# Kernel optimization log

Hardware: AMD Instinct MI355X
Metric: run time of the kernel (lower is better)

## Reference

```python
import jax, jax.numpy as jnp
import numpy as np

B, T, D, H = 4, 2048, 1024, 16
HD = D // H  # 64
LOCAL_CTX, BLOCKSIZE, VERTSIZE = 256, 1, 16
STRIDE = LOCAL_CTX // BLOCKSIZE  # 256


def build_fixed_mask(n):
    # num_verts == 1 branch of generate_fixed_attention_mask
    layout = np.zeros((n, n), dtype=np.bool_)
    # vertical stripes: top `vertsize` indices of each stride block
    for idx in range(STRIDE - VERTSIZE, STRIDE):
        layout[:, idx::STRIDE] = True
    rows = np.arange(n)
    # local: each query attends to its own stride-block
    same_block = (rows[:, None] // STRIDE) == (rows[None, :] // STRIDE)
    layout |= same_block
    # causal: zero out k > q
    layout &= rows[None, :] <= rows[:, None]
    return layout


def setup_inputs() -> dict:
    key = jax.random.key(0)
    k1, k2, k3, k4, k5 = jax.random.split(key, 5)
    s = 0.02
    return {
        "x": jax.random.normal(k1, (B, T, D), dtype=jnp.float32),
        "Wqkv": jax.random.normal(k2, (D, 3 * D), dtype=jnp.float32) * s,
        "bqkv": jax.random.normal(k3, (3 * D,), dtype=jnp.float32) * s,
        "Wproj": jax.random.normal(k4, (D, D), dtype=jnp.float32) * s,
        "bproj": jax.random.normal(k5, (D,), dtype=jnp.float32) * s,
        "mask": jnp.asarray(build_fixed_mask(T)),
    }


def reference(x, Wqkv, bqkv, Wproj, bproj, mask):
    b, t, _ = x.shape
    qkv = (x @ Wqkv + bqkv).reshape(b, t, 3, H, HD)
    # (B,T,3,H,HD) -> (B,H,T,HD) per component
    q = qkv[:, :, 0].transpose(0, 2, 1, 3)
    k = qkv[:, :, 1].transpose(0, 2, 1, 3)
    v = qkv[:, :, 2].transpose(0, 2, 1, 3)
    att = jnp.einsum("bhqd,bhkd->bhqk", q, k) * (1.0 / jnp.sqrt(jnp.float32(HD)))
    att = jnp.where(mask[:t, :t], att, -jnp.inf)
    att = jax.nn.softmax(att, axis=-1)
    y = jnp.einsum("bhqk,bhkd->bhqd", att, v)
    y = y.transpose(0, 2, 1, 3).reshape(b, t, D)
    return y @ Wproj + bproj
```

## Files before the change

kernel.cpp:

```cpp
#include <hip/hip_runtime.h>
#include <cstdint>
#include <cstddef>

typedef unsigned short u16;
typedef __attribute__((ext_vector_type(8))) short short8;
typedef __attribute__((ext_vector_type(4))) float f32x4;
typedef __attribute__((ext_vector_type(4))) unsigned short u16x4;

#define B_ 4
#define T_ 2048
#define D_ 1024
#define H_ 16
#define HD_ 64

__device__ __forceinline__ u16 f2bf(float f) {
  union { float f; unsigned i; } v; v.f = f;
  unsigned r = (v.i + 0x7FFFu + ((v.i >> 16) & 1u)) >> 16;
  return (u16)r;
}

__device__ __forceinline__ void load_lds16(const void* g, void* l) {
  __builtin_amdgcn_global_load_lds(
      (const __attribute__((address_space(1))) void*)g,
      (__attribute__((address_space(3))) void*)l, 16, 0, 0);
}

__global__ __launch_bounds__(256) void cvt_f32_bf16(const float* __restrict__ src,
                                                    u16* __restrict__ dst) {
  const size_t i = ((size_t)blockIdx.x * 256 + threadIdx.x) * 4;
  const f32x4 v = *(const f32x4*)(src + i);
  u16x4 o;
#pragma unroll
  for (int r = 0; r < 4; ++r) o[r] = f2bf(v[r]);
  *(u16x4*)(dst + i) = o;
}

__global__ __launch_bounds__(256) void transpose_cvt(const float* __restrict__ src,
                                                     u16* __restrict__ dst,
                                                     int R, int C) {
  __shared__ u16 t[32][33];
  const int c0 = blockIdx.x * 32, r0 = blockIdx.y * 32;
  const int tid = threadIdx.x;
  const int lr = tid >> 5, lc = tid & 31;
#pragma unroll
  for (int p = 0; p < 4; ++p)
    t[lr + p * 8][lc] = f2bf(src[(size_t)(r0 + lr + p * 8) * C + c0 + lc]);
  __syncthreads();
#pragma unroll
  for (int p = 0; p < 4; ++p)
    dst[(size_t)(c0 + lr + p * 8) * R + r0 + lc] = t[lc][lr + p * 8];
}

template <int EPI>
__global__ __launch_bounds__(256)
void gemm_bt(const u16* __restrict__ A, const u16* __restrict__ Bt,
             const float* __restrict__ bias, int K, int N,
             void* __restrict__ o0v, u16* __restrict__ o1, u16* __restrict__ o2) {
  __shared__ u16 As[128 * 32];
  __shared__ u16 Bs[128 * 32];
  const int tid = threadIdx.x;
  const int lane = tid & 63;
  const int w = tid >> 6;
  const int q = lane >> 4, col = lane & 15;
  const int m0 = blockIdx.y * 128, n0 = blockIdx.x * 128;
  const int wm = (w >> 1) * 64, wn = (w & 1) * 64;
  const int srow = tid >> 2, soff = (tid & 3) * 8;

  f32x4 acc[4][4] = {};

  const u16* Ap = A + (size_t)(m0 + srow) * K + soff;
  const u16* Bp = Bt + (size_t)(n0 + srow) * K + soff;

  for (int kb = 0; kb < K; kb += 32) {
    load_lds16(Ap + kb, &As[tid * 8]);
    load_lds16(Ap + (size_t)64 * K + kb, &As[2048 + tid * 8]);
    load_lds16(Bp + kb, &Bs[tid * 8]);
    load_lds16(Bp + (size_t)64 * K + kb, &Bs[2048 + tid * 8]);
    __syncthreads();
    short8 af[4], bfr[4];
#pragma unroll
    for (int i = 0; i < 4; ++i)
      af[i] = *(const short8*)&As[(wm + i * 16 + col) * 32 + q * 8];
#pragma unroll
    for (int j = 0; j < 4; ++j)
      bfr[j] = *(const short8*)&Bs[(wn + j * 16 + col) * 32 + q * 8];
#pragma unroll
    for (int i = 0; i < 4; ++i)
#pragma unroll
      for (int j = 0; j < 4; ++j)
        acc[i][j] = __builtin_amdgcn_mfma_f32_16x16x32_bf16(af[i], bfr[j], acc[i][j], 0, 0, 0);
    __syncthreads();
  }

#pragma unroll
  for (int j = 0; j < 4; ++j) {
    const int n = n0 + wn + j * 16 + col;
    const float bv = bias[n];
    if constexpr (EPI == 0) {
      u16* q0p = (u16*)o0v;
      const int c = n >> 10, rem = n & 1023, hh = rem >> 6, dd = rem & 63;
#pragma unroll
      for (int i = 0; i < 4; ++i) {
        const int mrow = m0 + wm + i * 16 + q * 4;
        const int b = mrow >> 11, t = mrow & 2047;
        const int bh = b * H_ + hh;
        if (c == 0) {
#pragma unroll
          for (int r = 0; r < 4; ++r)
            q0p[((size_t)bh * T_ + t + r) * HD_ + dd] = f2bf((acc[i][j][r] + bv) * 0.125f);
        } else if (c == 1) {
#pragma unroll
          for (int r = 0; r < 4; ++r)
            o1[((size_t)bh * T_ + t + r) * HD_ + dd] = f2bf(acc[i][j][r] + bv);
        } else {
          u16x4 pk;
#pragma unroll
          for (int r = 0; r < 4; ++r) pk[r] = f2bf(acc[i][j][r] + bv);
          *(u16x4*)&o2[((size_t)bh * HD_ + dd) * T_ + t] = pk;
        }
      }
    } else {
      float* outp = (float*)o0v;
#pragma unroll
      for (int i = 0; i < 4; ++i) {
        const int mrow = m0 + wm + i * 16 + q * 4;
#pragma unroll
        for (int r = 0; r < 4; ++r)
          outp[(size_t)(mrow + r) * N + n] = acc[i][j][r] + bv;
      }
    }
  }
}

__global__ __launch_bounds__(256)
void sparse_attn(const u16* __restrict__ Qb, const u16* __restrict__ Kb,
                 const u16* __restrict__ Vt, u16* __restrict__ Y) {
  __shared__ char smem[20480];
  u16* Pall = (u16*)smem;
  float* Obuf = (float*)smem;

  const int tid = threadIdx.x, lane = tid & 63, w = tid >> 6;
  const int q = lane >> 4, col = lane & 15;
  const int bh = blockIdx.y, qt = blockIdx.x;
  const int b = bh >> 4, hh = bh & 15;
  const int qb = qt >> 2;
  const int rb = (qt & 3) * 64;
  const int qg = qt * 64;
  const u16* Qh = Qb + (size_t)bh * T_ * HD_;
  const u16* Kh = Kb + (size_t)bh * T_ * HD_;
  const u16* Vh = Vt + (size_t)bh * HD_ * T_;

  short8 qf[4][2];
#pragma unroll
  for (int i = 0; i < 4; ++i)
#pragma unroll
    for (int h2 = 0; h2 < 2; ++h2)
      qf[i][h2] = *(const short8*)&Qh[(size_t)(qg + i * 16 + col) * HD_ + h2 * 32 + q * 8];

  f32x4 o[4][4] = {};
  f32x4 lI[4] = {};
  const short8 ones = {0x3F80, 0x3F80, 0x3F80, 0x3F80, 0x3F80, 0x3F80, 0x3F80, 0x3F80};

  u16* P = Pall + w * 2560;

  const int ns = (qb + 1) >> 1;
  const int L = ns + 2 * (qt & 3) + 2;

  for (int j = w; j < L; j += 4) {
    int k0, k1, localc;
    bool mask1;
    if (j < ns) {
      k0 = (2 * j) * 256 + 240; k1 = k0 + 256;
      mask1 = (2 * j + 1 == qb); localc = -1;
    } else {
      const int c = j - ns;
      k0 = qb * 256 + c * 32; k1 = k0 + 16;
      mask1 = false; localc = c * 32;
    }
    short8 k0a = *(const short8*)&Kh[(size_t)(k0 + col) * HD_ + q * 8];
    short8 k0b = *(const short8*)&Kh[(size_t)(k0 + col) * HD_ + 32 + q * 8];
    short8 k1a = *(const short8*)&Kh[(size_t)(k1 + col) * HD_ + q * 8];
    short8 k1b = *(const short8*)&Kh[(size_t)(k1 + col) * HD_ + 32 + q * 8];
#pragma unroll
    for (int rt = 0; rt < 4; ++rt) {
      f32x4 z = {0.f, 0.f, 0.f, 0.f};
      f32x4 s0 = __builtin_amdgcn_mfma_f32_16x16x32_bf16(qf[rt][0], k0a, z, 0, 0, 0);
      s0 = __builtin_amdgcn_mfma_f32_16x16x32_bf16(qf[rt][1], k0b, s0, 0, 0, 0);
      f32x4 s1 = __builtin_amdgcn_mfma_f32_16x16x32_bf16(qf[rt][0], k1a, z, 0, 0, 0);
      s1 = __builtin_amdgcn_mfma_f32_16x16x32_bf16(qf[rt][1], k1b, s1, 0, 0, 0);
#pragma unroll
      for (int r = 0; r < 4; ++r) {
        float p0 = __expf(s0[r]);
        float p1 = mask1 ? 0.f : __expf(s1[r]);
        if (localc >= 0) {
          const int qr = rb + rt * 16 + q * 4 + r;
          if (localc + col > qr) p0 = 0.f;
          if (localc + 16 + col > qr) p1 = 0.f;
        }
        P[(rt * 16 + q * 4 + r) * 40 + col] = f2bf(p0);
        P[(rt * 16 + q * 4 + r) * 40 + 16 + col] = f2bf(p1);
      }
    }
    asm volatile("s_waitcnt lgkmcnt(0)" ::: "memory");
    short8 pf[4], vf[4];
#pragma unroll
    for (int rt = 0; rt < 4; ++rt)
      pf[rt] = *(const short8*)&P[(rt * 16 + col) * 40 + q * 8];
    const int kvb = (q < 2) ? (k0 + q * 8) : (k1 + (q - 2) * 8);
#pragma unroll
    for (int dt = 0; dt < 4; ++dt)
      vf[dt] = *(const short8*)&Vh[(size_t)(dt * 16 + col) * T_ + kvb];
#pragma unroll
    for (int rt = 0; rt < 4; ++rt) {
#pragma unroll
      for (int dt = 0; dt < 4; ++dt)
        o[rt][dt] = __builtin_amdgcn_mfma_f32_16x16x32_bf16(pf[rt], vf[dt], o[rt][dt], 0, 0, 0);
      lI[rt] = __builtin_amdgcn_mfma_f32_16x16x32_bf16(pf[rt], ones, lI[rt], 0, 0, 0);
    }
  }

#pragma unroll
  for (int rt = 0; rt < 4; ++rt) {
    __syncthreads();
#pragma unroll
    for (int dt = 0; dt < 4; ++dt)
      *(f32x4*)&Obuf[(w * 65 + dt * 16 + col) * 16 + q * 4] = o[rt][dt];
    if (col == 0)
      *(f32x4*)&Obuf[(w * 65 + 64) * 16 + q * 4] = lI[rt];
    __syncthreads();
    f32x4 acc = {0.f, 0.f, 0.f, 0.f};
    f32x4 lt = {0.f, 0.f, 0.f, 0.f};
#pragma unroll
    for (int w2 = 0; w2 < 4; ++w2) {
      acc += *(const f32x4*)&Obuf[(w2 * 65 + w * 16 + col) * 16 + q * 4];
      lt += *(const f32x4*)&Obuf[(w2 * 65 + 64) * 16 + q * 4];
    }
#pragma unroll
    for (int r = 0; r < 4; ++r) {
      const int trow = qg + rt * 16 + q * 4 + r;
      Y[((size_t)(b * T_ + trow)) * D_ + hh * HD_ + w * 16 + col] = f2bf(acc[r] / lt[r]);
    }
  }
}

extern "C" void kernel_launch(void* const* d_in, const int* in_sizes, int n_in,
                              void* d_out, int out_size, void* d_ws, size_t ws_size,
                              hipStream_t stream) {
  const float* x = (const float*)d_in[0];
  const float* Wqkv = (const float*)d_in[1];
  const float* bqkv = (const float*)d_in[2];
  const float* Wproj = (const float*)d_in[3];
  const float* bproj = (const float*)d_in[4];
  float* out = (float*)d_out;

  char* ws = (char*)d_ws;
  u16* xb     = (u16*)(ws + 0);
  u16* WqkvT  = (u16*)(ws + 16777216);
  u16* WprojT = (u16*)(ws + 23068672);
  u16* Qb     = (u16*)(ws + 25165824);
  u16* Kb     = (u16*)(ws + 41943040);
  u16* Vt     = (u16*)(ws + 58720256);
  u16* Y      = (u16*)(ws + 75497472);

  cvt_f32_bf16<<<dim3(8192), 256, 0, stream>>>(x, xb);
  transpose_cvt<<<dim3(96, 32), 256, 0, stream>>>(Wqkv, WqkvT, 1024, 3072);
  transpose_cvt<<<dim3(32, 32), 256, 0, stream>>>(Wproj, WprojT, 1024, 1024);
  gemm_bt<0><<<dim3(24, 64), 256, 0, stream>>>(xb, WqkvT, bqkv, 1024, 3072, Qb, Kb, Vt);
  sparse_attn<<<dim3(32, 64), 256, 0, stream>>>(Qb, Kb, Vt, Y);
  gemm_bt<1><<<dim3(8, 64), 256, 0, stream>>>(Y, WprojT, bproj, 1024, 1024, out, nullptr, nullptr);
}
```

Measured before the change: 271.7 us.

## Replace GEMM with 256x256-tile, 4-stage LDS pipelined, swizzled MFMA kernel

Rewrites both projection GEMMs to use 256x256 output tiles with 512 threads. It uses a 4-buffer LDS ring that prefetches three K-tiles ahead via global_load_lds with fine-grained vmcnt waits, and XOR-swizzles LDS columns to avoid bank conflicts. Each wave computes a 128x64 sub-tile, with MFMA sections given raised priority. The aim is to hide global load latency and raise data reuse. In exchange it uses 128KB of LDS and many more accumulator registers, and produces fewer blocks (384 and 128), which may underfill the 256 CUs for the output projection.

```diff
diff --git a/kernel.cpp b/kernel.cpp
--- a/kernel.cpp
+++ b/kernel.cpp
@@ -52,45 +52,90 @@
 }
 
 template <int EPI>
-__global__ __launch_bounds__(256)
-void gemm_bt(const u16* __restrict__ A, const u16* __restrict__ Bt,
+__global__ __launch_bounds__(512, 2)
+void gemm256(const u16* __restrict__ A, const u16* __restrict__ Bt,
              const float* __restrict__ bias, int K, int N,
              void* __restrict__ o0v, u16* __restrict__ o1, u16* __restrict__ o2) {
-  __shared__ u16 As[128 * 32];
-  __shared__ u16 Bs[128 * 32];
+  __shared__ u16 tbuf[4 * 16384];
   const int tid = threadIdx.x;
   const int lane = tid & 63;
   const int w = tid >> 6;
   const int q = lane >> 4, col = lane & 15;
-  const int m0 = blockIdx.y * 128, n0 = blockIdx.x * 128;
-  const int wm = (w >> 1) * 64, wn = (w & 1) * 64;
-  const int srow = tid >> 2, soff = (tid & 3) * 8;
-
-  f32x4 acc[4][4] = {};
-
-  const u16* Ap = A + (size_t)(m0 + srow) * K + soff;
-  const u16* Bp = Bt + (size_t)(n0 + srow) * K + soff;
-
-  for (int kb = 0; kb < K; kb += 32) {
-    load_lds16(Ap + kb, &As[tid * 8]);
-    load_lds16(Ap + (size_t)64 * K + kb, &As[2048 + tid * 8]);
-    load_lds16(Bp + kb, &Bs[tid * 8]);
-    load_lds16(Bp + (size_t)64 * K + kb, &Bs[2048 + tid * 8]);
-    __syncthreads();
-    short8 af[4], bfr[4];
-#pragma unroll
-    for (int i = 0; i < 4; ++i)
-      af[i] = *(const short8*)&As[(wm + i * 16 + col) * 32 + q * 8];
-#pragma unroll
-    for (int j = 0; j < 4; ++j)
-      bfr[j] = *(const short8*)&Bs[(wn + j * 16 + col) * 32 + q * 8];
-#pragma unroll
-    for (int i = 0; i < 4; ++i)
-#pragma unroll
-      for (int j = 0; j < 4; ++j)
-        acc[i][j] = __builtin_amdgcn_mfma_f32_16x16x32_bf16(af[i], bfr[j], acc[i][j], 0, 0, 0);
-    __syncthreads();
-  }
+  const int m0 = blockIdx.y * 256, n0 = blockIdx.x * 256;
+  const int wm = (w >> 2) * 128, wn = (w & 3) * 64;
+
+  const int srow = tid >> 2;
+  const int scol = (((tid & 3) ^ ((tid >> 3) & 3)) << 3);
+  const u16* Ap = A + (size_t)(m0 + srow) * K + scol;
+  const u16* Bp = Bt + (size_t)(n0 + srow) * K + scol;
+  const size_t rstep = (size_t)128 * K;
+  const int NT = K >> 5;
+
+  f32x4 acc[8][4] = {};
+
+#pragma unroll
+  for (int t0 = 0; t0 < 3; ++t0) {
+    u16* dst = tbuf + t0 * 16384;
+    const int kb = t0 << 5;
+    load_lds16(Ap + kb, dst + tid * 8);
+    load_lds16(Ap + rstep + kb, dst + 4096 + tid * 8);
+    load_lds16(Bp + kb, dst + 8192 + tid * 8);
+    load_lds16(Bp + rstep + kb, dst + 12288 + tid * 8);
+  }
+  asm volatile("s_waitcnt vmcnt(8)" ::: "memory");
+  __builtin_amdgcn_s_barrier();
+
+  const int swz = ((q ^ ((col >> 1) & 3)) << 3);
+
+  for (int t = 0; t < NT; ++t) {
+    const u16* Ab = tbuf + (t & 3) * 16384;
+    const u16* Bb = Ab + 8192;
+    const int tp = t + 3;
+    u16* pdst = tbuf + (tp & 3) * 16384;
+    const bool pf = tp < NT;
+    const size_t kbp = (size_t)tp << 5;
+
+    short8 bfr[4];
+#pragma unroll
+    for (int p = 0; p < 2; ++p) {
+      short8 af[4];
+#pragma unroll
+      for (int i2 = 0; i2 < 4; ++i2)
+        af[i2] = *(const short8*)&Ab[(wm + (p * 4 + i2) * 16 + col) * 32 + swz];
+      if (p == 0) {
+#pragma unroll
+        for (int j = 0; j < 4; ++j)
+          bfr[j] = *(const short8*)&Bb[(wn + j * 16 + col) * 32 + swz];
+        if (pf) {
+          load_lds16(Ap + kbp, pdst + tid * 8);
+          load_lds16(Ap + rstep + kbp, pdst + 4096 + tid * 8);
+        }
+      } else if (pf) {
+        load_lds16(Bp + kbp, pdst + 8192 + tid * 8);
+        load_lds16(Bp + rstep + kbp, pdst + 12288 + tid * 8);
+      }
+      asm volatile("" ::: "memory");
+      __builtin_amdgcn_s_barrier();
+      asm volatile("s_waitcnt lgkmcnt(0)" ::: "memory");
+      __builtin_amdgcn_s_setprio(1);
+#pragma unroll
+      for (int i2 = 0; i2 < 4; ++i2)
+#pragma unroll
+        for (int j = 0; j < 4; ++j)
+          acc[p * 4 + i2][j] = __builtin_amdgcn_mfma_f32_16x16x32_bf16(af[i2], bfr[j], acc[p * 4 + i2][j], 0, 0, 0);
+      __builtin_amdgcn_s_setprio(0);
+      if (p == 1) {
+        if (t < NT - 3)       asm volatile("s_waitcnt vmcnt(8)" ::: "memory");
+        else if (t == NT - 3) asm volatile("s_waitcnt vmcnt(4)" ::: "memory");
+        else                  asm volatile("s_waitcnt vmcnt(0)" ::: "memory");
+      }
+      asm volatile("" ::: "memory");
+      __builtin_amdgcn_s_barrier();
+    }
+  }
+
+  asm volatile("s_waitcnt vmcnt(0)" ::: "memory");
+  asm volatile("" ::: "memory");
 
 #pragma unroll
   for (int j = 0; j < 4; ++j) {
@@ -100,29 +145,29 @@
       u16* q0p = (u16*)o0v;
       const int c = n >> 10, rem = n & 1023, hh = rem >> 6, dd = rem & 63;
 #pragma unroll
-      for (int i = 0; i < 4; ++i) {
+      for (int i = 0; i < 8; ++i) {
         const int mrow = m0 + wm + i * 16 + q * 4;
-        const int b = mrow >> 11, t = mrow & 2047;
+        const int b = mrow >> 11, t2 = mrow & 2047;
         const int bh = b * H_ + hh;
         if (c == 0) {
 #pragma unroll
           for (int r = 0; r < 4; ++r)
-            q0p[((size_t)bh * T_ + t + r) * HD_ + dd] = f2bf((acc[i][j][r] + bv) * 0.125f);
+            q0p[((size_t)bh * T_ + t2 + r) * HD_ + dd] = f2bf((acc[i][j][r] + bv) * 0.125f);
         } else if (c == 1) {
 #pragma unroll
           for (int r = 0; r < 4; ++r)
-            o1[((size_t)bh * T_ + t + r) * HD_ + dd] = f2bf(acc[i][j][r] + bv);
+            o1[((size_t)bh * T_ + t2 + r) * HD_ + dd] = f2bf(acc[i][j][r] + bv);
         } else {
           u16x4 pk;
 #pragma unroll
           for (int r = 0; r < 4; ++r) pk[r] = f2bf(acc[i][j][r] + bv);
-          *(u16x4*)&o2[((size_t)bh * HD_ + dd) * T_ + t] = pk;
+          *(u16x4*)&o2[((size_t)bh * HD_ + dd) * T_ + t2] = pk;
         }
       }
     } else {
       float* outp = (float*)o0v;
 #pragma unroll
-      for (int i = 0; i < 4; ++i) {
+      for (int i = 0; i < 8; ++i) {
         const int mrow = m0 + wm + i * 16 + q * 4;
 #pragma unroll
         for (int r = 0; r < 4; ++r)
@@ -265,7 +310,7 @@
   cvt_f32_bf16<<<dim3(8192), 256, 0, stream>>>(x, xb);
   transpose_cvt<<<dim3(96, 32), 256, 0, stream>>>(Wqkv, WqkvT, 1024, 3072);
   transpose_cvt<<<dim3(32, 32), 256, 0, stream>>>(Wproj, WprojT, 1024, 1024);
-  gemm_bt<0><<<dim3(24, 64), 256, 0, stream>>>(xb, WqkvT, bqkv, 1024, 3072, Qb, Kb, Vt);
+  gemm256<0><<<dim3(12, 32), 512, 0, stream>>>(xb, WqkvT, bqkv, 1024, 3072, Qb, Kb, Vt);
   sparse_attn<<<dim3(32, 64), 256, 0, stream>>>(Qb, Kb, Vt, Y);
-  gemm_bt<1><<<dim3(8, 64), 256, 0, stream>>>(Y, WprojT, bproj, 1024, 1024, out, nullptr, nullptr);
-}
+  gemm256<1><<<dim3(4, 32), 512, 0, stream>>>(Y, WprojT, bproj, 1024, 1024, out, nullptr, nullptr);
+}
```

Result: slower. 279.3 us (+2.8%).

## Replace GEMMs with 256x256 8-wave double-buffered pipelined kernel

Applied to the files above, without the earlier changes.

Replaces the simple 128x128 GEMM, which had a single LDS buffer and synchronous loads, with a 512-thread kernel using 256x256 tiles. K tiles of 64 are double-buffered in a swizzled LDS layout, async loads are interleaved with MFMA phases, and vmcnt waits are placed explicitly. It also adds a block-id remap for L2 locality and raises MFMA priority with setprio. The aim is to hide global load latency and improve reuse per tile. The cost is 128KB of LDS per block and fewer blocks in flight (384 and 128 workgroups), which may leave CUs underused for the smaller projection GEMM.

```diff
diff --git a/kernel.cpp b/kernel.cpp
--- a/kernel.cpp
+++ b/kernel.cpp
@@ -24,6 +24,9 @@
       (const __attribute__((address_space(1))) void*)g,
       (__attribute__((address_space(3))) void*)l, 16, 0, 0);
 }
+
+#define BAR() __builtin_amdgcn_s_barrier()
+#define VMC(n) asm volatile("s_waitcnt vmcnt(" #n ")" ::: "memory")
 
 __global__ __launch_bounds__(256) void cvt_f32_bf16(const float* __restrict__ src,
                                                     u16* __restrict__ dst) {
@@ -52,81 +55,145 @@
 }
 
 template <int EPI>
-__global__ __launch_bounds__(256)
-void gemm_bt(const u16* __restrict__ A, const u16* __restrict__ Bt,
-             const float* __restrict__ bias, int K, int N,
-             void* __restrict__ o0v, u16* __restrict__ o1, u16* __restrict__ o2) {
-  __shared__ u16 As[128 * 32];
-  __shared__ u16 Bs[128 * 32];
+__global__ __launch_bounds__(512, 2)
+void gemm8p(const u16* __restrict__ A, const u16* __restrict__ Bt,
+            const float* __restrict__ bias, int K, int N,
+            void* __restrict__ o0v, u16* __restrict__ o1, u16* __restrict__ o2) {
+  __shared__ u16 tbuf[65536];
   const int tid = threadIdx.x;
   const int lane = tid & 63;
   const int w = tid >> 6;
   const int q = lane >> 4, col = lane & 15;
-  const int m0 = blockIdx.y * 128, n0 = blockIdx.x * 128;
-  const int wm = (w >> 1) * 64, wn = (w & 1) * 64;
-  const int srow = tid >> 2, soff = (tid & 3) * 8;
-
-  f32x4 acc[4][4] = {};
-
-  const u16* Ap = A + (size_t)(m0 + srow) * K + soff;
-  const u16* Bp = Bt + (size_t)(n0 + srow) * K + soff;
-
-  for (int kb = 0; kb < K; kb += 32) {
-    load_lds16(Ap + kb, &As[tid * 8]);
-    load_lds16(Ap + (size_t)64 * K + kb, &As[2048 + tid * 8]);
-    load_lds16(Bp + kb, &Bs[tid * 8]);
-    load_lds16(Bp + (size_t)64 * K + kb, &Bs[2048 + tid * 8]);
-    __syncthreads();
-    short8 af[4], bfr[4];
+
+  const int nbx = gridDim.x;
+  const int id = blockIdx.y * nbx + blockIdx.x;
+  const int nwg = nbx * gridDim.y;
+  const int sid = (id & 7) * (nwg >> 3) + (id >> 3);
+  const int m0 = (sid / nbx) * 256, n0 = (sid % nbx) * 256;
+
+  const int c8 = ((lane & 7) ^ (lane >> 3)) * 8;
+  const size_t go0 = (size_t)(w * 16 + (lane >> 3)) * K + c8;
+  const size_t go1 = (size_t)(w * 16 + 8 + (lane >> 3)) * K + c8;
+  const int d0 = w * 1024 + lane * 8, d1 = d0 + 512;
+
+  auto STAGE = [&](int isB, int buf, int half, int tile) {
+    const u16* s = isB ? Bt : A;
+    const u16* g = s + (size_t)((isB ? n0 : m0) + half * 128) * K + ((size_t)tile << 6);
+    u16* d = tbuf + (isB ? 32768 : 0) + (buf * 2 + half) * 8192;
+    load_lds16(g + go0, d + d0);
+    load_lds16(g + go1, d + d1);
+  };
+
+  short8 af[4][2], bfr[2][2];
+  const int arow = (w >> 2) * 64 + col;
+  const int brow = (w & 3) * 32 + col;
+  const int sA0 = ((0 * 4 + q) ^ (col & 7)) * 8, sA1 = ((1 * 4 + q) ^ (col & 7)) * 8;
+
+  auto LDA = [&](int buf, int pm) {
+    const u16* base = tbuf + (buf * 2 + pm) * 8192;
+#pragma unroll
+    for (int i = 0; i < 4; ++i) {
+      af[i][0] = *(const short8*)&base[(arow + i * 16) * 64 + sA0];
+      af[i][1] = *(const short8*)&base[(arow + i * 16) * 64 + sA1];
+    }
+  };
+  auto LDB = [&](int buf, int pn) {
+    const u16* base = tbuf + 32768 + (buf * 2 + pn) * 8192;
+#pragma unroll
+    for (int j = 0; j < 2; ++j) {
+      bfr[j][0] = *(const short8*)&base[(brow + j * 16) * 64 + sA0];
+      bfr[j][1] = *(const short8*)&base[(brow + j * 16) * 64 + sA1];
+    }
+  };
+
+  f32x4 acc[8][4] = {};
+  auto MM = [&](int pm, int pn) {
+    __builtin_amdgcn_s_setprio(1);
 #pragma unroll
     for (int i = 0; i < 4; ++i)
-      af[i] = *(const short8*)&As[(wm + i * 16 + col) * 32 + q * 8];
-#pragma unroll
-    for (int j = 0; j < 4; ++j)
-      bfr[j] = *(const short8*)&Bs[(wn + j * 16 + col) * 32 + q * 8];
-#pragma unroll
-    for (int i = 0; i < 4; ++i)
-#pragma unroll
-      for (int j = 0; j < 4; ++j)
-        acc[i][j] = __builtin_amdgcn_mfma_f32_16x16x32_bf16(af[i], bfr[j], acc[i][j], 0, 0, 0);
-    __syncthreads();
+#pragma unroll
+      for (int j = 0; j < 2; ++j) {
+        acc[pm * 4 + i][pn * 2 + j] =
+            __builtin_amdgcn_mfma_f32_16x16x32_bf16(af[i][0], bfr[j][0], acc[pm * 4 + i][pn * 2 + j], 0, 0, 0);
+        acc[pm * 4 + i][pn * 2 + j] =
+            __builtin_amdgcn_mfma_f32_16x16x32_bf16(af[i][1], bfr[j][1], acc[pm * 4 + i][pn * 2 + j], 0, 0, 0);
+      }
+    __builtin_amdgcn_s_setprio(0);
+  };
+
+  const int NI = K >> 7;
+
+  STAGE(0, 0, 0, 0); STAGE(0, 0, 1, 0); STAGE(1, 0, 0, 0); STAGE(1, 0, 1, 0);
+  STAGE(0, 1, 0, 1); STAGE(0, 1, 1, 1); STAGE(1, 1, 0, 1);
+  VMC(0);
+  BAR();
+
+  for (int i = 0; i < NI; ++i) {
+    const int t1 = 2 * i + 1, t2 = 2 * i + 2, t3 = 2 * i + 3;
+    const bool pf = (i < NI - 1);
+    LDA(0, 0); LDB(0, 0);
+    STAGE(1, 1, 1, t1);
+    BAR(); MM(0, 0); BAR();
+    LDB(0, 1);
+    if (pf) STAGE(0, 0, 0, t2);
+    BAR(); MM(0, 1); BAR();
+    LDA(0, 1); LDB(0, 0);
+    BAR(); MM(1, 0); BAR();
+    LDB(0, 1);
+    if (pf) { STAGE(1, 0, 0, t2); STAGE(0, 0, 1, t2); }
+    BAR(); MM(1, 1);
+    if (pf) { VMC(6); } else { VMC(0); }
+    BAR();
+    LDA(1, 0); LDB(1, 0);
+    if (pf) STAGE(1, 0, 1, t2);
+    BAR(); MM(0, 0); BAR();
+    LDB(1, 1);
+    if (pf) STAGE(0, 1, 0, t3);
+    BAR(); MM(0, 1); BAR();
+    LDA(1, 1); LDB(1, 0);
+    BAR(); MM(1, 0); BAR();
+    LDB(1, 1);
+    if (pf) { STAGE(1, 1, 0, t3); STAGE(0, 1, 1, t3); }
+    BAR(); MM(1, 1);
+    if (pf) { VMC(6); }
+    BAR();
   }
 
 #pragma unroll
-  for (int j = 0; j < 4; ++j) {
-    const int n = n0 + wn + j * 16 + col;
+  for (int bj = 0; bj < 4; ++bj) {
+    const int n = n0 + (w & 3) * 32 + (bj >> 1) * 128 + (bj & 1) * 16 + col;
     const float bv = bias[n];
     if constexpr (EPI == 0) {
       u16* q0p = (u16*)o0v;
       const int c = n >> 10, rem = n & 1023, hh = rem >> 6, dd = rem & 63;
 #pragma unroll
-      for (int i = 0; i < 4; ++i) {
-        const int mrow = m0 + wm + i * 16 + q * 4;
-        const int b = mrow >> 11, t = mrow & 2047;
+      for (int a = 0; a < 8; ++a) {
+        const int mrow = m0 + (w >> 2) * 64 + (a >> 2) * 128 + (a & 3) * 16 + q * 4;
+        const int b = mrow >> 11, t2r = mrow & 2047;
         const int bh = b * H_ + hh;
         if (c == 0) {
 #pragma unroll
           for (int r = 0; r < 4; ++r)
-            q0p[((size_t)bh * T_ + t + r) * HD_ + dd] = f2bf((acc[i][j][r] + bv) * 0.125f);
+            q0p[((size_t)bh * T_ + t2r + r) * HD_ + dd] = f2bf((acc[a][bj][r] + bv) * 0.125f);
         } else if (c == 1) {
 #pragma unroll
           for (int r = 0; r < 4; ++r)
-            o1[((size_t)bh * T_ + t + r) * HD_ + dd] = f2bf(acc[i][j][r] + bv);
+            o1[((size_t)bh * T_ + t2r + r) * HD_ + dd] = f2bf(acc[a][bj][r] + bv);
         } else {
           u16x4 pk;
 #pragma unroll
-          for (int r = 0; r < 4; ++r) pk[r] = f2bf(acc[i][j][r] + bv);
-          *(u16x4*)&o2[((size_t)bh * HD_ + dd) * T_ + t] = pk;
+          for (int r = 0; r < 4; ++r) pk[r] = f2bf(acc[a][bj][r] + bv);
+          *(u16x4*)&o2[((size_t)bh * HD_ + dd) * T_ + t2r] = pk;
         }
       }
     } else {
       float* outp = (float*)o0v;
 #pragma unroll
-      for (int i = 0; i < 4; ++i) {
-        const int mrow = m0 + wm + i * 16 + q * 4;
+      for (int a = 0; a < 8; ++a) {
+        const int mrow = m0 + (w >> 2) * 64 + (a >> 2) * 128 + (a & 3) * 16 + q * 4;
 #pragma unroll
         for (int r = 0; r < 4; ++r)
-          outp[(size_t)(mrow + r) * N + n] = acc[i][j][r] + bv;
+          outp[(size_t)(mrow + r) * N + n] = acc[a][bj][r] + bv;
       }
     }
   }
@@ -265,7 +332,7 @@
   cvt_f32_bf16<<<dim3(8192), 256, 0, stream>>>(x, xb);
   transpose_cvt<<<dim3(96, 32), 256, 0, stream>>>(Wqkv, WqkvT, 1024, 3072);
   transpose_cvt<<<dim3(32, 32), 256, 0, stream>>>(Wproj, WprojT, 1024, 1024);
-  gemm_bt<0><<<dim3(24, 64), 256, 0, stream>>>(xb, WqkvT, bqkv, 1024, 3072, Qb, Kb, Vt);
+  gemm8p<0><<<dim3(12, 32), 512, 0, stream>>>(xb, WqkvT, bqkv, 1024, 3072, Qb, Kb, Vt);
   sparse_attn<<<dim3(32, 64), 256, 0, stream>>>(Qb, Kb, Vt, Y);
-  gemm_bt<1><<<dim3(8, 64), 256, 0, stream>>>(Y, WprojT, bproj, 1024, 1024, out, nullptr, nullptr);
-}
+  gemm8p<1><<<dim3(4, 32), 512, 0, stream>>>(Y, WprojT, bproj, 1024, 1024, out, nullptr, nullptr);
+}
```

After: 273.5 us. About the same (+0.7%).
